# Performance work log

Hardware: AMD Instinct MI355X
Metric: run time of the kernel (lower is better)

## Reference

```python
import jax, jax.numpy as jnp
import numpy as np

NA = 3        # num anchors
NM = 32       # num prototype masks
NC = 80       # num classes
STRIDE = 8    # network stride
THRESH = 0.05 # conf threshold


def setup_inputs() -> dict:
    key = jax.random.key(0)
    nB, nH, nW = 16, 80, 80
    channels = NA * (5 + NC) + NA * NM  # 351
    output = jax.random.normal(key, (nB, channels, nH, nW), dtype=jnp.float32)
    # anchors already in output-grid units (pixel anchors / stride), shape [NA, 2] = (w, h)
    anchors = jnp.array([[1.25, 1.625], [2.0, 3.75], [4.125, 2.875]], dtype=jnp.float32)
    return {"output": output, "anchors": anchors}


def reference(output, anchors):
    nB, channels, nH, nW = output.shape
    nHW = nH * nW
    # split box head and mask-coefficient head
    box = output[:, :NA * (5 + NC)].reshape(nB, NA, 5 + NC, nHW)
    mask_out = output[:, NA * (5 + NC):].reshape(nB, NA, NM, nHW).transpose(0, 1, 3, 2)  # [nB,NA,nHW,NM]

    lin_y, lin_x = jnp.meshgrid(jnp.arange(nH, dtype=output.dtype),
                                jnp.arange(nW, dtype=output.dtype), indexing='ij')
    lin_x = lin_x.reshape(-1)
    lin_y = lin_y.reshape(-1)

    anchor_wh = anchors.reshape(1, NA, 2, 1)  # broadcast over [nB,NA,2,nHW]
    max_value = jnp.floor(jnp.log(jnp.asarray(1e35, output.dtype) / anchors.max() / STRIDE))

    xs = jax.nn.sigmoid(box[:, :, 0]) + lin_x                                   # [nB,NA,nHW]
    ys = jax.nn.sigmoid(box[:, :, 1]) + lin_y                                   # [nB,NA,nHW]
    wh = jnp.exp(jnp.minimum(box[:, :, 2:4], max_value)) * anchor_wh            # [nB,NA,2,nHW]
    obj = jax.nn.sigmoid(box[:, :, 4])                                          # [nB,NA,nHW]

    cls = jax.nn.softmax(box[:, :, 5:], axis=2)                                 # [nB,NA,NC,nHW]
    cls_max = cls.max(axis=2)
    cls_idx = cls.argmax(axis=2).astype(output.dtype)
    score = cls_max * obj                                                        # [nB,NA,nHW]

    keep = score > THRESH
    b, a, p = jnp.nonzero(keep)  # eager: data-dependent detection count N

    coords = jnp.stack([xs[b, a, p], ys[b, a, p], wh[b, a, 0, p], wh[b, a, 1, p]], axis=1) * STRIDE  # [N,4]
    mc = mask_out[b, a, p]                                                        # [N,NM]
    return jnp.concatenate([
        b[:, None].astype(output.dtype),
        coords,
        mc,
        score[b, a, p][:, None],
        cls_idx[b, a, p][:, None],
    ], axis=1)  # [N, 7+NM]
```

## Files before the change

### kernel.cpp

```cpp
#include <hip/hip_runtime.h>
#include <math.h>

#define NA 3
#define NM 32
#define NC 80
#define STRIDE_PX 8.0f
#define THRESH 0.05f
#define NB 16
#define NH 80
#define NW 80
#define NHW (NH * NW)
#define CH (NA * (5 + NC) + NA * NM)
#define BOXCH (NA * (5 + NC))
#define TOTAL (NB * NA * NHW)
#define BLK 256
#define NBLK (TOTAL / BLK)
#define ROWSZ (7 + NM)
#define WS_ROW_STRIDE (BLK * ROWSZ)

__device__ __forceinline__ int wave_sum64(int v) {
#pragma unroll
  for (int s = 32; s > 0; s >>= 1) v += __shfl_xor(v, s, 64);
  return v;
}

__global__ __launch_bounds__(BLK) void decode_kernel(
    const float* __restrict__ in, const float* __restrict__ anchors,
    float* __restrict__ wsrows, int* __restrict__ counts) {
  int g = blockIdx.x * BLK + threadIdx.x;
  int p = g % NHW;
  int a = (g / NHW) % NA;
  int b = g / (NA * NHW);

  const float* base = in + ((size_t)b * CH + (size_t)a * (5 + NC)) * NHW + p;

  float tx = base[0];
  float ty = base[(size_t)1 * NHW];
  float tw = base[(size_t)2 * NHW];
  float th = base[(size_t)3 * NHW];
  float tobj = base[(size_t)4 * NHW];

  float m = -INFINITY, s = 0.f;
  int idx = 0;
#pragma unroll
  for (int j = 0; j < NC; ++j) {
    float x = base[(size_t)(5 + j) * NHW];
    float mn = fmaxf(m, x);
    s = s * __expf(m - mn) + __expf(x - mn);
    idx = (x > m) ? j : idx;
    m = mn;
  }

  float cls_max = 1.0f / s;
  float obj = 1.0f / (1.0f + __expf(-tobj));
  float score = cls_max * obj;

  float amax = fmaxf(fmaxf(fmaxf(anchors[0], anchors[1]), fmaxf(anchors[2], anchors[3])),
                     fmaxf(anchors[4], anchors[5]));
  float max_value = floorf(logf(1e35f / amax / STRIDE_PX));
  float aw = anchors[a * 2 + 0];
  float ah = anchors[a * 2 + 1];

  float xs = 1.0f / (1.0f + __expf(-tx)) + (float)(p % NW);
  float ys = 1.0f / (1.0f + __expf(-ty)) + (float)(p / NW);
  float w = __expf(fminf(tw, max_value)) * aw;
  float h = __expf(fminf(th, max_value)) * ah;

  bool keep = score > THRESH;
  unsigned long long ball = __ballot(keep);
  int lane = threadIdx.x & 63;
  int wv = threadIdx.x >> 6;
  int lower = __popcll(ball & ((1ull << lane) - 1ull));
  __shared__ int wc[BLK / 64];
  if (lane == 0) wc[wv] = __popcll(ball);
  __syncthreads();
  int pre = 0;
#pragma unroll
  for (int i = 0; i < BLK / 64; ++i)
    if (i < wv) pre += wc[i];

  if (keep) {
    int lrank = pre + lower;
    float* o = wsrows + (size_t)blockIdx.x * WS_ROW_STRIDE + (size_t)lrank * ROWSZ;
    o[0] = (float)b;
    o[1] = xs * STRIDE_PX;
    o[2] = ys * STRIDE_PX;
    o[3] = w * STRIDE_PX;
    o[4] = h * STRIDE_PX;
    const float* mbase = in + ((size_t)b * CH + BOXCH + (size_t)a * NM) * NHW + p;
#pragma unroll
    for (int mm = 0; mm < NM; ++mm) o[5 + mm] = mbase[(size_t)mm * NHW];
    o[5 + NM] = score;
    o[6 + NM] = (float)idx;
  }
  if (threadIdx.x == 0)
    counts[blockIdx.x] = wc[0] + wc[1] + wc[2] + wc[3];
}

__global__ __launch_bounds__(BLK) void emit_kernel(
    const float* __restrict__ wsrows, const int* __restrict__ counts,
    float* __restrict__ out, int out_size) {
  int bid = blockIdx.x;
  int t = threadIdx.x;

  int partial = 0;
  for (int j = t; j < bid; j += BLK) partial += counts[j];
  partial = wave_sum64(partial);
  __shared__ int sh[BLK / 64];
  if ((t & 63) == 0) sh[t >> 6] = partial;
  __syncthreads();
  int off = sh[0] + sh[1] + sh[2] + sh[3];

  int cnt = counts[bid];
  int nelem = cnt * ROWSZ;
  const float* src = wsrows + (size_t)bid * WS_ROW_STRIDE;
  int dbase = off * ROWSZ;
  for (int e = t; e < nelem; e += BLK) {
    int d = dbase + e;
    if (d < out_size) out[d] = src[e];
  }
}

extern "C" void kernel_launch(void* const* d_in, const int* in_sizes, int n_in,
                              void* d_out, int out_size, void* d_ws, size_t ws_size,
                              hipStream_t stream) {
  const float* in = (const float*)d_in[0];
  const float* anchors = (const float*)d_in[1];

  float* wsrows = (float*)d_ws;
  int* counts = (int*)((float*)d_ws + (size_t)NBLK * WS_ROW_STRIDE);

  decode_kernel<<<NBLK, BLK, 0, stream>>>(in, anchors, wsrows, counts);
  emit_kernel<<<NBLK, BLK, 0, stream>>>(wsrows, counts, (float*)d_out, out_size);
}
```

Measured before the change: 225.2 us.

## Vectorize decode to float4 per thread with single-wave blocks

Each decode thread now processes four consecutive cells, using 128-bit float4 loads for the box, class and mask channels. Blocks shrink to one 64-lane wave that covers the same 256 cells, so compaction uses per-wave ballots with no shared memory or block barrier. Mask coefficients are read with vector loads for all four cells, even cells that are not kept, and scattered into the workspace rows. The aim is fewer memory instructions and better bandwidth on this load-bound kernel, at the cost of more registers per thread and fewer threads in flight.

```diff
diff --git a/kernel.cpp b/kernel.cpp
--- a/kernel.cpp
+++ b/kernel.cpp
@@ -13,10 +13,14 @@
 #define CH (NA * (5 + NC) + NA * NM)
 #define BOXCH (NA * (5 + NC))
 #define TOTAL (NB * NA * NHW)
-#define BLK 256
-#define NBLK (TOTAL / BLK)
+#define CPB 256
+#define BPA (NHW / CPB)
+#define NBLK (TOTAL / CPB)
 #define ROWSZ (7 + NM)
-#define WS_ROW_STRIDE (BLK * ROWSZ)
+#define WS_ROW_STRIDE (CPB * ROWSZ)
+#define EBLK 256
+
+typedef float f4 __attribute__((ext_vector_type(4)));
 
 __device__ __forceinline__ int wave_sum64(int v) {
 #pragma unroll
@@ -24,36 +28,37 @@
   return v;
 }
 
-__global__ __launch_bounds__(BLK) void decode_kernel(
+__global__ __launch_bounds__(64) void decode_kernel(
     const float* __restrict__ in, const float* __restrict__ anchors,
     float* __restrict__ wsrows, int* __restrict__ counts) {
-  int g = blockIdx.x * BLK + threadIdx.x;
-  int p = g % NHW;
-  int a = (g / NHW) % NA;
-  int b = g / (NA * NHW);
+  const int t = threadIdx.x;
+  const int bid = blockIdx.x;
+  const int b = bid / (NA * BPA);
+  const int a = (bid / BPA) % NA;
+  const int pbase = (bid % BPA) * CPB + t * 4;
 
-  const float* base = in + ((size_t)b * CH + (size_t)a * (5 + NC)) * NHW + p;
+  const float* base = in + ((size_t)b * CH + (size_t)a * (5 + NC)) * NHW + pbase;
 
-  float tx = base[0];
-  float ty = base[(size_t)1 * NHW];
-  float tw = base[(size_t)2 * NHW];
-  float th = base[(size_t)3 * NHW];
-  float tobj = base[(size_t)4 * NHW];
+  f4 tx = *(const f4*)(base + (size_t)0 * NHW);
+  f4 ty = *(const f4*)(base + (size_t)1 * NHW);
+  f4 tw = *(const f4*)(base + (size_t)2 * NHW);
+  f4 th = *(const f4*)(base + (size_t)3 * NHW);
+  f4 tob = *(const f4*)(base + (size_t)4 * NHW);
 
-  float m = -INFINITY, s = 0.f;
-  int idx = 0;
+  f4 m = {-INFINITY, -INFINITY, -INFINITY, -INFINITY};
+  f4 s = {0.f, 0.f, 0.f, 0.f};
+  int idx[4] = {0, 0, 0, 0};
 #pragma unroll
   for (int j = 0; j < NC; ++j) {
-    float x = base[(size_t)(5 + j) * NHW];
-    float mn = fmaxf(m, x);
-    s = s * __expf(m - mn) + __expf(x - mn);
-    idx = (x > m) ? j : idx;
-    m = mn;
+    f4 x = *(const f4*)(base + (size_t)(5 + j) * NHW);
+#pragma unroll
+    for (int k = 0; k < 4; ++k) {
+      float mn = fmaxf(m[k], x[k]);
+      s[k] = s[k] * __expf(m[k] - mn) + __expf(x[k] - mn);
+      idx[k] = (x[k] > m[k]) ? j : idx[k];
+      m[k] = mn;
+    }
   }
-
-  float cls_max = 1.0f / s;
-  float obj = 1.0f / (1.0f + __expf(-tobj));
-  float score = cls_max * obj;
 
   float amax = fmaxf(fmaxf(fmaxf(anchors[0], anchors[1]), fmaxf(anchors[2], anchors[3])),
                      fmaxf(anchors[4], anchors[5]));
@@ -61,52 +66,71 @@
   float aw = anchors[a * 2 + 0];
   float ah = anchors[a * 2 + 1];
 
-  float xs = 1.0f / (1.0f + __expf(-tx)) + (float)(p % NW);
-  float ys = 1.0f / (1.0f + __expf(-ty)) + (float)(p / NW);
-  float w = __expf(fminf(tw, max_value)) * aw;
-  float h = __expf(fminf(th, max_value)) * ah;
+  bool keep[4];
+  float xs[4], ys[4], ww[4], hh[4], sc[4];
+#pragma unroll
+  for (int k = 0; k < 4; ++k) {
+    float cls_max = 1.0f / s[k];
+    float obj = 1.0f / (1.0f + __expf(-tob[k]));
+    sc[k] = cls_max * obj;
+    int p = pbase + k;
+    xs[k] = 1.0f / (1.0f + __expf(-tx[k])) + (float)(p % NW);
+    ys[k] = 1.0f / (1.0f + __expf(-ty[k])) + (float)(p / NW);
+    ww[k] = __expf(fminf(tw[k], max_value)) * aw;
+    hh[k] = __expf(fminf(th[k], max_value)) * ah;
+    keep[k] = sc[k] > THRESH;
+  }
 
-  bool keep = score > THRESH;
-  unsigned long long ball = __ballot(keep);
-  int lane = threadIdx.x & 63;
-  int wv = threadIdx.x >> 6;
-  int lower = __popcll(ball & ((1ull << lane) - 1ull));
-  __shared__ int wc[BLK / 64];
-  if (lane == 0) wc[wv] = __popcll(ball);
-  __syncthreads();
-  int pre = 0;
+  unsigned long long lowm = (1ull << t) - 1ull;
+  unsigned long long ball[4];
+  int below = 0, tot = 0;
 #pragma unroll
-  for (int i = 0; i < BLK / 64; ++i)
-    if (i < wv) pre += wc[i];
+  for (int k = 0; k < 4; ++k) {
+    ball[k] = __ballot(keep[k]);
+    below += __popcll(ball[k] & lowm);
+    tot += __popcll(ball[k]);
+  }
+  if (t == 0) counts[bid] = tot;
 
-  if (keep) {
-    int lrank = pre + lower;
-    float* o = wsrows + (size_t)blockIdx.x * WS_ROW_STRIDE + (size_t)lrank * ROWSZ;
-    o[0] = (float)b;
-    o[1] = xs * STRIDE_PX;
-    o[2] = ys * STRIDE_PX;
-    o[3] = w * STRIDE_PX;
-    o[4] = h * STRIDE_PX;
-    const float* mbase = in + ((size_t)b * CH + BOXCH + (size_t)a * NM) * NHW + p;
+  int rk[4], r = below;
 #pragma unroll
-    for (int mm = 0; mm < NM; ++mm) o[5 + mm] = mbase[(size_t)mm * NHW];
-    o[5 + NM] = score;
-    o[6 + NM] = (float)idx;
+  for (int k = 0; k < 4; ++k) { rk[k] = r; r += keep[k] ? 1 : 0; }
+
+  float* slab = wsrows + (size_t)bid * WS_ROW_STRIDE;
+#pragma unroll
+  for (int k = 0; k < 4; ++k) {
+    if (keep[k]) {
+      float* o = slab + (size_t)rk[k] * ROWSZ;
+      o[0] = (float)b;
+      o[1] = xs[k] * STRIDE_PX;
+      o[2] = ys[k] * STRIDE_PX;
+      o[3] = ww[k] * STRIDE_PX;
+      o[4] = hh[k] * STRIDE_PX;
+      o[5 + NM] = sc[k];
+      o[6 + NM] = (float)idx[k];
+    }
   }
-  if (threadIdx.x == 0)
-    counts[blockIdx.x] = wc[0] + wc[1] + wc[2] + wc[3];
+
+  const float* mbase = in + ((size_t)b * CH + BOXCH + (size_t)a * NM) * NHW + pbase;
+#pragma unroll
+  for (int mm = 0; mm < NM; ++mm) {
+    f4 mv = *(const f4*)(mbase + (size_t)mm * NHW);
+#pragma unroll
+    for (int k = 0; k < 4; ++k)
+      if (keep[k]) slab[(size_t)rk[k] * ROWSZ + 5 + mm] = mv[k];
+  }
 }
 
-__global__ __launch_bounds__(BLK) void emit_kernel(
+__global__ __launch_bounds__(EBLK) void emit_kernel(
     const float* __restrict__ wsrows, const int* __restrict__ counts,
     float* __restrict__ out, int out_size) {
   int bid = blockIdx.x;
   int t = threadIdx.x;
 
   int partial = 0;
-  for (int j = t; j < bid; j += BLK) partial += counts[j];
+  for (int j = t; j < bid; j += EBLK) partial += counts[j];
   partial = wave_sum64(partial);
-  __shared__ int sh[BLK / 64];
+  __shared__ int sh[EBLK / 64];
   if ((t & 63) == 0) sh[t >> 6] = partial;
   __syncthreads();
   int off = sh[0] + sh[1] + sh[2] + sh[3];
@@ -115,7 +139,7 @@
   int nelem = cnt * ROWSZ;
   const float* src = wsrows + (size_t)bid * WS_ROW_STRIDE;
   int dbase = off * ROWSZ;
-  for (int e = t; e < nelem; e += BLK) {
+  for (int e = t; e < nelem; e += EBLK) {
     int d = dbase + e;
     if (d < out_size) out[d] = src[e];
   }
@@ -130,6 +154,6 @@
   float* wsrows = (float*)d_ws;
   int* counts = (int*)((float*)d_ws + (size_t)NBLK * WS_ROW_STRIDE);
 
-  decode_kernel<<<NBLK, BLK, 0, stream>>>(in, anchors, wsrows, counts);
-  emit_kernel<<<NBLK, BLK, 0, stream>>>(wsrows, counts, (float*)d_out, out_size);
+  decode_kernel<<<NBLK, 64, 0, stream>>>(in, anchors, wsrows, counts);
+  emit_kernel<<<NBLK, EBLK, 0, stream>>>(wsrows, counts, (float*)d_out, out_size);
 }
```

New measurement: 403.2 us. +79.1%, slower.

## Stage kept detection rows in LDS and write slabs with vector stores

Applied to the files above, without the earlier changes.

Decode now builds each block's compacted detection rows in shared memory and copies them to the workspace slab with coalesced float4 stores, instead of scattered per-thread global writes. Mask-coefficient channels are loaded by all threads in batches of eight, rather than only by kept threads. The class-logit loop is restructured into batches of eight loads with the outer loop not unrolled. This trades extra global reads of the mask channels and more LDS use for coalesced output writes.

```diff
diff --git a/kernel.cpp b/kernel.cpp
--- a/kernel.cpp
+++ b/kernel.cpp
@@ -14,9 +14,14 @@
 #define BOXCH (NA * (5 + NC))
 #define TOTAL (NB * NA * NHW)
 #define BLK 256
-#define NBLK (TOTAL / BLK)
+#define CPB 256
+#define BPA (NHW / CPB)
+#define NBLK (TOTAL / CPB)
 #define ROWSZ (7 + NM)
-#define WS_ROW_STRIDE (BLK * ROWSZ)
+#define WS_ROW_STRIDE (CPB * ROWSZ)
+#define EBLK 256
+
+typedef float f4 __attribute__((ext_vector_type(4)));
 
 __device__ __forceinline__ int wave_sum64(int v) {
 #pragma unroll
@@ -27,10 +32,14 @@
 __global__ __launch_bounds__(BLK) void decode_kernel(
     const float* __restrict__ in, const float* __restrict__ anchors,
     float* __restrict__ wsrows, int* __restrict__ counts) {
-  int g = blockIdx.x * BLK + threadIdx.x;
-  int p = g % NHW;
-  int a = (g / NHW) % NA;
-  int b = g / (NA * NHW);
+  __shared__ float rows[CPB * ROWSZ];
+  __shared__ int wc[BLK / 64];
+
+  const int t = threadIdx.x;
+  const int bid = blockIdx.x;
+  const int b = bid / (NA * BPA);
+  const int a = (bid / BPA) % NA;
+  const int p = (bid % BPA) * CPB + t;
 
   const float* base = in + ((size_t)b * CH + (size_t)a * (5 + NC)) * NHW + p;
 
@@ -42,13 +51,20 @@
 
   float m = -INFINITY, s = 0.f;
   int idx = 0;
+#pragma unroll 1
+  for (int jb = 0; jb < NC; jb += 8) {
+    float xv[8];
 #pragma unroll
-  for (int j = 0; j < NC; ++j) {
-    float x = base[(size_t)(5 + j) * NHW];
-    float mn = fmaxf(m, x);
-    s = s * __expf(m - mn) + __expf(x - mn);
-    idx = (x > m) ? j : idx;
-    m = mn;
+    for (int u = 0; u < 8; ++u)
+      xv[u] = base[(size_t)(5 + jb + u) * NHW];
+#pragma unroll
+    for (int u = 0; u < 8; ++u) {
+      float x = xv[u];
+      float mn = fmaxf(m, x);
+      s = s * __expf(m - mn) + __expf(x - mn);
+      idx = (x > m) ? (jb + u) : idx;
+      m = mn;
+    }
   }
 
   float cls_max = 1.0f / s;
@@ -68,45 +84,65 @@
 
   bool keep = score > THRESH;
   unsigned long long ball = __ballot(keep);
-  int lane = threadIdx.x & 63;
-  int wv = threadIdx.x >> 6;
+  int lane = t & 63;
+  int wv = t >> 6;
   int lower = __popcll(ball & ((1ull << lane) - 1ull));
-  __shared__ int wc[BLK / 64];
   if (lane == 0) wc[wv] = __popcll(ball);
   __syncthreads();
   int pre = 0;
 #pragma unroll
   for (int i = 0; i < BLK / 64; ++i)
     if (i < wv) pre += wc[i];
+  int cnt = wc[0] + wc[1] + wc[2] + wc[3];
+  int rk = pre + lower;
 
   if (keep) {
-    int lrank = pre + lower;
-    float* o = wsrows + (size_t)blockIdx.x * WS_ROW_STRIDE + (size_t)lrank * ROWSZ;
+    float* o = rows + rk * ROWSZ;
     o[0] = (float)b;
     o[1] = xs * STRIDE_PX;
     o[2] = ys * STRIDE_PX;
     o[3] = w * STRIDE_PX;
     o[4] = h * STRIDE_PX;
-    const float* mbase = in + ((size_t)b * CH + BOXCH + (size_t)a * NM) * NHW + p;
-#pragma unroll
-    for (int mm = 0; mm < NM; ++mm) o[5 + mm] = mbase[(size_t)mm * NHW];
     o[5 + NM] = score;
     o[6 + NM] = (float)idx;
   }
-  if (threadIdx.x == 0)
-    counts[blockIdx.x] = wc[0] + wc[1] + wc[2] + wc[3];
+
+  const float* mbase = in + ((size_t)b * CH + BOXCH + (size_t)a * NM) * NHW + p;
+#pragma unroll 1
+  for (int mb = 0; mb < NM; mb += 8) {
+    float mv[8];
+#pragma unroll
+    for (int u = 0; u < 8; ++u)
+      mv[u] = mbase[(size_t)(mb + u) * NHW];
+    if (keep) {
+#pragma unroll
+      for (int u = 0; u < 8; ++u)
+        rows[rk * ROWSZ + 5 + mb + u] = mv[u];
+    }
+  }
+
+  if (t == 0) counts[bid] = cnt;
+  __syncthreads();
+
+  float* slab = wsrows + (size_t)bid * WS_ROW_STRIDE;
+  int nelem = cnt * ROWSZ;
+  int n4 = nelem >> 2;
+  f4* slab4 = (f4*)slab;
+  const f4* rows4 = (const f4*)rows;
+  for (int e = t; e < n4; e += BLK) slab4[e] = rows4[e];
+  for (int e = (n4 << 2) + t; e < nelem; e += BLK) slab[e] = rows[e];
 }
 
-__global__ __launch_bounds__(BLK) void emit_kernel(
+__global__ __launch_bounds__(EBLK) void emit_kernel(
     const float* __restrict__ wsrows, const int* __restrict__ counts,
     float* __restrict__ out, int out_size) {
   int bid = blockIdx.x;
   int t = threadIdx.x;
 
   int partial = 0;
-  for (int j = t; j < bid; j += BLK) partial += counts[j];
+  for (int j = t; j < bid; j += EBLK) partial += counts[j];
   partial = wave_sum64(partial);
-  __shared__ int sh[BLK / 64];
+  __shared__ int sh[EBLK / 64];
   if ((t & 63) == 0) sh[t >> 6] = partial;
   __syncthreads();
   int off = sh[0] + sh[1] + sh[2] + sh[3];
@@ -115,7 +151,7 @@
   int nelem = cnt * ROWSZ;
   const float* src = wsrows + (size_t)bid * WS_ROW_STRIDE;
   int dbase = off * ROWSZ;
-  for (int e = t; e < nelem; e += BLK) {
+  for (int e = t; e < nelem; e += EBLK) {
     int d = dbase + e;
     if (d < out_size) out[d] = src[e];
   }
@@ -131,5 +167,5 @@
   int* counts = (int*)((float*)d_ws + (size_t)NBLK * WS_ROW_STRIDE);
 
   decode_kernel<<<NBLK, BLK, 0, stream>>>(in, anchors, wsrows, counts);
-  emit_kernel<<<NBLK, BLK, 0, stream>>>(wsrows, counts, (float*)d_out, out_size);
+  emit_kernel<<<NBLK, EBLK, 0, stream>>>(wsrows, counts, (float*)d_out, out_size);
 }
```

Measured after the change: 227.4 us. About the same (+1.0%).
